# Optimization experiments

Hardware: AMD Instinct MI355X
Metric: run time of the kernel (lower is better)

Reference implementation:

```python
import jax, jax.numpy as jnp
import numpy as np

HEADS = 8

def setup_inputs() -> dict:
    key = jax.random.key(0)
    ks = jax.random.split(key, 10)
    B, S, E = 2, 2048, 512
    q = jax.random.normal(ks[0], (B, S, E), jnp.float32)
    k = jax.random.normal(ks[1], (B, S, E), jnp.float32)
    v = jax.random.normal(ks[2], (B, S, E), jnp.float32)
    mask = jnp.zeros((S, S), jnp.float32)  # additive mask [s_q, s_k]
    scale = 0.02
    Wq = jax.random.normal(ks[3], (E, E), jnp.float32) * scale
    bq = jax.random.normal(ks[4], (E,), jnp.float32) * scale
    Wk = jax.random.normal(ks[5], (E, E), jnp.float32) * scale
    bk = jax.random.normal(ks[6], (E,), jnp.float32) * scale
    Wv = jax.random.normal(ks[7], (E, E), jnp.float32) * scale
    bv = jax.random.normal(ks[8], (E,), jnp.float32) * scale
    return {"q": q, "k": k, "v": v, "mask": mask,
            "Wq": Wq, "bq": bq, "Wk": Wk, "bk": bk, "Wv": Wv, "bv": bv}

def reference(q, k, v, mask, Wq, bq, Wk, bk, Wv, bv):
    H = HEADS
    b, s_q, _ = q.shape
    s_k = k.shape[1]
    s_v = v.shape[1]
    # NOTE: faithful to source: row-major view(b, H, s, -1) WITHOUT transposing
    # seq/head axes first (quirk of the original module).
    K = jnp.swapaxes((k @ Wk.T + bk).reshape(b, H, s_k, -1), 2, 3)  # [b,H,dh,s_k]
    Q = (q @ Wq.T + bq).reshape(b, H, s_q, -1)                      # [b,H,s_q,dh]
    V = (v @ Wv.T + bv).reshape(b, H, s_v, -1)                      # [b,H,s_v,dh]
    # NOTE: original scales by sqrt(K.shape[-1]) AFTER the transpose, i.e. sqrt(s_k)
    scores = (Q @ K) / jnp.sqrt(jnp.asarray(s_k, jnp.float32))      # [b,H,s_q,s_k]
    scores = scores + mask[:s_q, :s_k]
    attn = jax.nn.softmax(scores, axis=-1)
    out = (attn @ V).reshape(b, s_q, -1)  # [b, s_q, e]
    return out
```

## Files before the change

kernel.cpp:

```cpp
#include <hip/hip_runtime.h>


#define SEQ 2048
#define EMB 512
#define DH  64
#define MROWS 4096
#define NROWS 32768

typedef float  v4f __attribute__((ext_vector_type(4)));
typedef short  v8s __attribute__((ext_vector_type(8)));
typedef __fp16 v2h __attribute__((ext_vector_type(2)));

static __device__ __forceinline__ unsigned int f2bf(float f) {
    unsigned int u = __float_as_uint(f);
    u += 0x7fffu + ((u >> 16) & 1u);
    return u >> 16;
}
static __device__ __forceinline__ unsigned int pack2(float a, float b) {
    return f2bf(a) | (f2bf(b) << 16);
}
static __device__ __forceinline__ unsigned int packh2(float a, float b) {
    v2h h = __builtin_amdgcn_cvt_pkrtz(a, b);
    return __builtin_bit_cast(unsigned int, h);
}

__global__ __launch_bounds__(256, 3) void proj_kernel(
    const float* __restrict__ q, const float* __restrict__ k, const float* __restrict__ v,
    const float* __restrict__ Wq, const float* __restrict__ bq,
    const float* __restrict__ Wk, const float* __restrict__ bk,
    const float* __restrict__ Wv, const float* __restrict__ bv,
    const float* __restrict__ mask,
    unsigned short* __restrict__ Qbf, unsigned short* __restrict__ Kbf,
    unsigned short* __restrict__ Vbf, float* __restrict__ maskT)
{
    const int tid = threadIdx.x;

    if (blockIdx.x >= 768) {
        const int mb2 = blockIdx.x - 768;
        const int rb = mb2 >> 5, kt = mb2 & 31;
        float* tile = maskT + ((size_t)rb * 32 + kt) * 8192;
#pragma unroll
        for (int i = 0; i < 8; ++i) {
            int s = tid + i * 256;
            int l  = s & 63;
            int cb = (s >> 6) & 3;
            int g  = (s >> 8) & 1;
            int w  = (s >> 9) & 3;
            int qd = l >> 4, n = l & 15;
            float4 f = *(const float4*)&mask[
                (size_t)(rb * 128 + w * 32 + g * 16 + n) * SEQ + kt * 64 + cb * 16 + qd * 4];
            *(float4*)&tile[(size_t)s * 4] = f;
        }
        return;
    }

    __shared__ __align__(16) char smem[27648];
    char* As = smem;
    char* Ws = smem + 9216;

    const int id  = blockIdx.x;
    const int pos = id & 31;
    const int nb  = pos >> 3;
    const int unit = (id >> 5) * 8 + (pos & 7);
    const int mb = unit & 63;
    const int z  = unit >> 6;

    const float* A    = (z == 0) ? q  : (z == 1) ? k  : v;
    const float* W    = (z == 0) ? Wq : (z == 1) ? Wk : Wv;
    const float* bias = (z == 0) ? bq : (z == 1) ? bk : bv;
    unsigned short* Cg = (z == 0) ? Qbf : (z == 1) ? Kbf : Vbf;

    const int w    = tid >> 6;
    const int lane = tid & 63;
    const int qd   = lane >> 4;
    const int n    = lane & 15;
    const int m0 = mb * 64, n0 = nb * 128;

    float4 areg[4], wreg[8];
#pragma unroll
    for (int i = 0; i < 4; ++i) {
        int c = tid + i * 256;
        areg[i] = *(const float4*)&A[(size_t)(m0 + (c >> 4)) * EMB + (c & 15) * 4];
    }
#pragma unroll
    for (int i = 0; i < 8; ++i) {
        int c = tid + i * 256;
        wreg[i] = *(const float4*)&W[(size_t)(n0 + (c >> 4)) * EMB + (c & 15) * 4];
    }

    v4f acc[8];
#pragma unroll
    for (int cb = 0; cb < 8; ++cb) acc[cb] = (v4f)0.f;

#pragma unroll 1
    for (int kt = 0; kt < 8; ++kt) {
        __syncthreads();
#pragma unroll
        for (int i = 0; i < 4; ++i) {
            int c = tid + i * 256;
            uint2 pk = { pack2(areg[i].x, areg[i].y), pack2(areg[i].z, areg[i].w) };
            *(uint2*)&As[(c >> 4) * 144 + (c & 15) * 8] = pk;
        }
#pragma unroll
        for (int i = 0; i < 8; ++i) {
            int c = tid + i * 256;
            uint2 pk = { pack2(wreg[i].x, wreg[i].y), pack2(wreg[i].z, wreg[i].w) };
            *(uint2*)&Ws[(c >> 4) * 144 + (c & 15) * 8] = pk;
        }
        __syncthreads();

        if (kt + 1 < 8) {
#pragma unroll
            for (int i = 0; i < 4; ++i) {
                int c = tid + i * 256;
                areg[i] = *(const float4*)&A[(size_t)(m0 + (c >> 4)) * EMB + (kt+1) * 64 + (c & 15) * 4];
            }
#pragma unroll
            for (int i = 0; i < 8; ++i) {
                int c = tid + i * 256;
                wreg[i] = *(const float4*)&W[(size_t)(n0 + (c >> 4)) * EMB + (kt+1) * 64 + (c & 15) * 4];
            }
        }

#pragma unroll
        for (int ks = 0; ks < 2; ++ks) {
            v8s af = *(const v8s*)&As[(w * 16 + n) * 144 + ks * 64 + qd * 16];
#pragma unroll
            for (int cb = 0; cb < 8; ++cb) {
                v8s bfr = *(const v8s*)&Ws[(cb * 16 + n) * 144 + ks * 64 + qd * 16];
                acc[cb] = __builtin_amdgcn_mfma_f32_16x16x32_bf16(af, bfr, acc[cb], 0, 0, 0);
            }
        }
    }

    const float osc = (z == 0) ? 0.02209708691207961f : 1.0f;
    float bb[8];
#pragma unroll
    for (int cb = 0; cb < 8; ++cb) bb[cb] = bias[n0 + cb * 16 + n];
#pragma unroll
    for (int cb = 0; cb < 8; ++cb)
#pragma unroll
        for (int r = 0; r < 4; ++r) acc[cb][r] = (acc[cb][r] + bb[cb]) * osc;

    __syncthreads();
    short* Ct = (short*)smem;
#pragma unroll
    for (int cb = 0; cb < 8; ++cb)
#pragma unroll
        for (int r = 0; r < 4; ++r)
            Ct[(w * 16 + qd * 4 + r) * 136 + cb * 16 + n] = (short)f2bf(acc[cb][r]);
    __syncthreads();
    const int rr = tid >> 2, q4 = tid & 3;
#pragma unroll
    for (int i = 0; i < 4; ++i) {
        uint4 t4 = *(const uint4*)&smem[rr * 272 + q4 * 64 + i * 16];
        *(uint4*)&Cg[(size_t)(m0 + rr) * EMB + n0 + q4 * 32 + i * 8] = t4;
    }
}

__global__ __launch_bounds__(256) void vtrans_kernel(
    const unsigned short* __restrict__ Vbf, unsigned short* __restrict__ VtT)
{
    __shared__ unsigned short T[64 * 136];
    const int bh = blockIdx.x, kt = blockIdx.y;
    const int tid = threadIdx.x;
    const unsigned short* Vh = Vbf + (size_t)bh * (SEQ * DH) + (size_t)kt * 64 * DH;
#pragma unroll
    for (int i = 0; i < 2; ++i) {
        int c = tid + i * 256;
        int s_l = c >> 3, ch = c & 7;
        uint4 t4 = *(const uint4*)&Vh[c * 8];
        const unsigned short* e = (const unsigned short*)&t4;
#pragma unroll
        for (int j = 0; j < 8; ++j)
            T[(ch * 8 + j) * 136 + s_l] = e[j];
    }
    __syncthreads();
    unsigned short* Ot = VtT + ((size_t)bh * 32 + kt) * (64 * 64);
    const int d = tid >> 2, sq = tid & 3;
#pragma unroll
    for (int i = 0; i < 2; ++i) {
        uint4 t4 = *(const uint4*)&T[d * 136 + sq * 16 + i * 8];
        *(uint4*)&Ot[d * 64 + sq * 16 + i * 8] = t4;
    }
}

template <int SPLITS>
__global__ __launch_bounds__(256, 4) void attn_kernel(
    const unsigned short* __restrict__ Qbf, const unsigned short* __restrict__ Kbf,
    const unsigned short* __restrict__ VtT,
    const float* __restrict__ maskT, const float* __restrict__ maskf,
    unsigned short* __restrict__ Opart, float* __restrict__ ml,
    float* __restrict__ out)
{
    __shared__ __align__(16) char smem[36864];
    char* Ks  = smem;
    char* Vts = smem + 9216;

    const int tid  = threadIdx.x;
    const int w    = tid >> 6;
    const int lane = tid & 63;
    const int qd   = lane >> 4;
    const int n    = lane & 15;
    char* Ps = smem + 18432 + w * 4608;

    const int id = blockIdx.x;
    const int rb = ((id >> 3) & 1) * 8 + (id & 7);
    const int bh = (id >> 4) & 15;
    const int kq = id >> 8;
    const int KT0 = kq * (32 / SPLITS), KT1 = KT0 + 32 / SPLITS;

    const unsigned short* Qh = Qbf + (size_t)bh * (SEQ * DH);
    const unsigned short* Kh = Kbf + (size_t)bh * (SEQ * DH);
    const unsigned short* Vth = VtT + (size_t)bh * 32 * 4096;

    v8s qf[2][2];
#pragma unroll
    for (int g = 0; g < 2; ++g) {
        const size_t qrow = (size_t)(rb * 128 + w * 32 + g * 16 + n);
#pragma unroll
        for (int ks = 0; ks < 2; ++ks)
            qf[g][ks] = *(const v8s*)&Qh[qrow * DH + ks * 32 + qd * 8];
    }

    uint4 kreg[2], vreg[2];
#pragma unroll
    for (int p = 0; p < 2; ++p) {
        int c = tid + p * 256;
        kreg[p] = *(const uint4*)&Kh[(size_t)KT0 * 4096 + c * 8];
        vreg[p] = *(const uint4*)&Vth[(size_t)KT0 * 4096 + c * 8];
    }

    float l_[2] = { 0.f, 0.f };
    v4f oacc[2][4];
#pragma unroll
    for (int g = 0; g < 2; ++g)
#pragma unroll
        for (int cb = 0; cb < 4; ++cb) oacc[g][cb] = (v4f)0.f;

#pragma unroll 1
    for (int kt = KT0; kt < KT1; ++kt) {
        __syncthreads();
#pragma unroll
        for (int p = 0; p < 2; ++p) {
            int c = tid + p * 256;
            *(uint4*)&Ks [(c >> 3) * 144 + (c & 7) * 16] = kreg[p];
            *(uint4*)&Vts[(c >> 3) * 144 + (c & 7) * 16] = vreg[p];
        }
        __syncthreads();

        v4f sacc[2][4];
        float4 mk[2][4];
        if (SPLITS > 1) {
            const float* tileF = maskT + ((size_t)rb * 32 + kt) * 8192;
#pragma unroll
            for (int g = 0; g < 2; ++g)
#pragma unroll
                for (int cb = 0; cb < 4; ++cb)
                    sacc[g][cb] = *(const v4f*)&tileF[
                        (size_t)((((w * 2 + g) * 4 + cb) * 64) + qd * 16 + n) * 4];
        } else {
#pragma unroll
            for (int g = 0; g < 2; ++g) {
                const size_t mrow = (size_t)(rb * 128 + w * 32 + g * 16 + n);
#pragma unroll
                for (int cb = 0; cb < 4; ++cb) {
                    mk[g][cb] = *(const float4*)&maskf[mrow * SEQ + kt * 64 + cb * 16 + qd * 4];
                    sacc[g][cb] = (v4f)0.f;
                }
            }
        }

        if (kt + 1 < KT1) {
#pragma unroll
            for (int p = 0; p < 2; ++p) {
                int c = tid + p * 256;
                kreg[p] = *(const uint4*)&Kh[(size_t)(kt + 1) * 4096 + c * 8];
                vreg[p] = *(const uint4*)&Vth[(size_t)(kt + 1) * 4096 + c * 8];
            }
        }

#pragma unroll
        for (int ks = 0; ks < 2; ++ks)
#pragma unroll
            for (int cb = 0; cb < 4; ++cb) {
                v8s kf = *(const v8s*)&Ks[(cb * 16 + n) * 144 + ks * 64 + qd * 16];
#pragma unroll
                for (int g = 0; g < 2; ++g)
                    sacc[g][cb] = __builtin_amdgcn_mfma_f32_16x16x32_bf16(kf, qf[g][ks], sacc[g][cb], 0, 0, 0);
            }

#pragma unroll
        for (int g = 0; g < 2; ++g) {
            float rs = 0.f;
            float pv[4][4];
#pragma unroll
            for (int cb = 0; cb < 4; ++cb) {
                if (SPLITS == 1) {
                    sacc[g][cb][0] += mk[g][cb].x; sacc[g][cb][1] += mk[g][cb].y;
                    sacc[g][cb][2] += mk[g][cb].z; sacc[g][cb][3] += mk[g][cb].w;
                }
#pragma unroll
                for (int r = 0; r < 4; ++r) {
                    float e = __expf(sacc[g][cb][r]);
                    pv[cb][r] = e;
                    rs += e;
                }
            }
            rs += __shfl_xor(rs, 16);
            rs += __shfl_xor(rs, 32);
            l_[g] += rs;
#pragma unroll
            for (int cb = 0; cb < 4; ++cb) {
                uint2 pk = { pack2(pv[cb][0], pv[cb][1]), pack2(pv[cb][2], pv[cb][3]) };
                *(uint2*)&Ps[(g * 16 + n) * 144 + cb * 32 + qd * 8] = pk;
            }
        }

#pragma unroll
        for (int ks = 0; ks < 2; ++ks) {
            v8s pf[2];
#pragma unroll
            for (int g = 0; g < 2; ++g)
                pf[g] = *(const v8s*)&Ps[(g * 16 + n) * 144 + ks * 64 + qd * 16];
#pragma unroll
            for (int cb = 0; cb < 4; ++cb) {
                v8s vf = *(const v8s*)&Vts[(cb * 16 + n) * 144 + ks * 64 + qd * 16];
#pragma unroll
                for (int g = 0; g < 2; ++g)
                    oacc[g][cb] = __builtin_amdgcn_mfma_f32_16x16x32_bf16(vf, pf[g], oacc[g][cb], 0, 0, 0);
            }
        }
    }

    if (SPLITS == 1) {
#pragma unroll
        for (int g = 0; g < 2; ++g) {
            const float inv = 1.0f / l_[g];
#pragma unroll
            for (int cb = 0; cb < 4; ++cb)
#pragma unroll
                for (int r = 0; r < 4; ++r) oacc[g][cb][r] *= inv;
        }
    } else {
        if (qd == 0) {
#pragma unroll
            for (int g = 0; g < 2; ++g) {
                const size_t row = (size_t)bh * SEQ + rb * 128 + w * 32 + g * 16 + n;
                ml[(size_t)kq * NROWS + row] = l_[g];
            }
        }
    }
    __syncthreads();
#pragma unroll
    for (int g = 0; g < 2; ++g)
#pragma unroll
        for (int cb = 0; cb < 4; ++cb)
            *(v4f*)&smem[(w * 32 + g * 16 + n) * 272 + cb * 64 + qd * 16] = oacc[g][cb];
    __syncthreads();
    const int r_l = tid >> 1, hf = tid & 1;
    if (SPLITS == 1) {
        float* dst = &out[((size_t)bh * SEQ + rb * 128 + r_l) * DH + hf * 32];
#pragma unroll
        for (int i = 0; i < 8; ++i) {
            float4 t4 = *(const float4*)&smem[r_l * 272 + hf * 128 + i * 16];
            *(float4*)&dst[i * 4] = t4;
        }
    } else {
        unsigned short* dst = &Opart[((size_t)kq * NROWS + (size_t)bh * SEQ + rb * 128 + r_l) * DH + hf * 32];
#pragma unroll
        for (int i = 0; i < 4; ++i) {
            float4 f0 = *(const float4*)&smem[r_l * 272 + hf * 128 + i * 32];
            float4 f1 = *(const float4*)&smem[r_l * 272 + hf * 128 + i * 32 + 16];
            uint4 o = { packh2(f0.x, f0.y), packh2(f0.z, f0.w),
                        packh2(f1.x, f1.y), packh2(f1.z, f1.w) };
            *(uint4*)&dst[i * 8] = o;
        }
    }
}

__global__ __launch_bounds__(256) void combine_kernel(
    const unsigned int* __restrict__ Opart, const float* __restrict__ ml,
    float* __restrict__ out, int splits)
{
    const int tid = threadIdx.x;
    const size_t row = (size_t)blockIdx.x * 16 + (tid >> 4);
    const int d4 = (tid & 15) * 4;
    float denom = 0.f;
    float4 o = make_float4(0.f, 0.f, 0.f, 0.f);
    for (int s = 0; s < splits; ++s) {
        denom += ml[(size_t)s * NROWS + row];
        uint2 u = *(const uint2*)&Opart[((size_t)s * NROWS + row) * 32 + (d4 >> 1)];
        v2h h0 = __builtin_bit_cast(v2h, u.x);
        v2h h1 = __builtin_bit_cast(v2h, u.y);
        o.x += (float)h0.x; o.y += (float)h0.y;
        o.z += (float)h1.x; o.w += (float)h1.y;
    }
    const float inv = 1.0f / denom;
    o.x *= inv; o.y *= inv; o.z *= inv; o.w *= inv;
    *(float4*)&out[row * DH + d4] = o;
}

extern "C" void kernel_launch(void* const* d_in, const int* in_sizes, int n_in,
                              void* d_out, int out_size, void* d_ws, size_t ws_size,
                              hipStream_t stream) {
    const float* q    = (const float*)d_in[0];
    const float* k    = (const float*)d_in[1];
    const float* v    = (const float*)d_in[2];
    const float* mask = (const float*)d_in[3];
    const float* Wq   = (const float*)d_in[4];
    const float* bq   = (const float*)d_in[5];
    const float* Wk   = (const float*)d_in[6];
    const float* bk   = (const float*)d_in[7];
    const float* Wv   = (const float*)d_in[8];
    const float* bv   = (const float*)d_in[9];

    char* ws = (char*)d_ws;
    const size_t MB = 1024 * 1024;
    unsigned short* Qbf   = (unsigned short*)(ws + 0);
    unsigned short* Kbf   = (unsigned short*)(ws + 4 * MB);
    unsigned short* VtT   = (unsigned short*)(ws + 8 * MB);
    unsigned short* Opart = (unsigned short*)(ws + 12 * MB);
    unsigned short* Vbf   = (unsigned short*)(ws + 12 * MB);
    float*          mlp   = (float*)(ws + 28 * MB);
    float*          maskT = (float*)(ws + 29 * MB);

    const size_t need_split = 45 * MB;
    const bool do_split = ws_size >= need_split;

    if (do_split) {
        proj_kernel<<<1280, 256, 0, stream>>>(q, k, v, Wq, bq, Wk, bk, Wv, bv,
                                              mask, Qbf, Kbf, Vbf, maskT);
        dim3 tgrid(16, 32);
        vtrans_kernel<<<tgrid, 256, 0, stream>>>(Vbf, VtT);
        attn_kernel<4><<<1024, 256, 0, stream>>>(Qbf, Kbf, VtT, maskT, mask,
                                                 Opart, mlp, (float*)d_out);
        combine_kernel<<<NROWS / 16, 256, 0, stream>>>((const unsigned int*)Opart,
                                                       mlp, (float*)d_out, 4);
    } else {
        proj_kernel<<<768, 256, 0, stream>>>(q, k, v, Wq, bq, Wk, bk, Wv, bv,
                                             mask, Qbf, Kbf, Vbf, maskT);
        dim3 tgrid(16, 32);
        vtrans_kernel<<<tgrid, 256, 0, stream>>>(Vbf, VtT);
        attn_kernel<1><<<256, 256, 0, stream>>>(Qbf, Kbf, VtT, maskT, mask,
                                                Opart, mlp, (float*)d_out);
    }
}
```

Baseline: 180.6 us.

## Pass P through ds_bpermute instead of LDS and halve shared memory

Softmax probabilities are now moved from the S-accumulator layout into the MFMA B-operand layout with ds_bpermute lane shuffles, so the per-wave P buffer in shared memory is no longer needed. The output epilogue is split into two passes over g so that it fits in the smaller buffer. Shared memory use drops from 36 KB to 18 KB and the launch bound rises to 6 blocks per CU to raise occupancy. The cost is eight bpermutes per g and ks, an extra pair of barriers in the epilogue, and tighter register limits that may cause spills.

```diff
diff --git a/kernel.cpp b/kernel.cpp
--- a/kernel.cpp
+++ b/kernel.cpp
@@ -186,14 +186,14 @@
 }
 
 template <int SPLITS>
-__global__ __launch_bounds__(256, 4) void attn_kernel(
+__global__ __launch_bounds__(256, 6) void attn_kernel(
     const unsigned short* __restrict__ Qbf, const unsigned short* __restrict__ Kbf,
     const unsigned short* __restrict__ VtT,
     const float* __restrict__ maskT, const float* __restrict__ maskf,
     unsigned short* __restrict__ Opart, float* __restrict__ ml,
     float* __restrict__ out)
 {
-    __shared__ __align__(16) char smem[36864];
+    __shared__ __align__(16) char smem[18432];
     char* Ks  = smem;
     char* Vts = smem + 9216;
 
@@ -202,7 +202,6 @@
     const int lane = tid & 63;
     const int qd   = lane >> 4;
     const int n    = lane & 15;
-    char* Ps = smem + 18432 + w * 4608;
 
     const int id = blockIdx.x;
     const int rb = ((id >> 3) & 1) * 8 + (id & 7);
@@ -214,6 +213,10 @@
     const unsigned short* Kh = Kbf + (size_t)bh * (SEQ * DH);
     const unsigned short* Vth = VtT + (size_t)bh * 32 * 4096;
 
+    const int aL1 = ((((2 * qd) & 3) * 16) + n) * 4;
+    const int aL2 = ((((2 * qd + 1) & 3) * 16) + n) * 4;
+    const bool hi = (qd >= 2);
+
     v8s qf[2][2];
 #pragma unroll
     for (int g = 0; g < 2; ++g) {
@@ -290,6 +293,7 @@
                     sacc[g][cb] = __builtin_amdgcn_mfma_f32_16x16x32_bf16(kf, qf[g][ks], sacc[g][cb], 0, 0, 0);
             }
 
+        v8s pf[2][2];
 #pragma unroll
         for (int g = 0; g < 2; ++g) {
             float rs = 0.f;
@@ -310,27 +314,38 @@
             rs += __shfl_xor(rs, 16);
             rs += __shfl_xor(rs, 32);
             l_[g] += rs;
-#pragma unroll
-            for (int cb = 0; cb < 4; ++cb) {
-                uint2 pk = { pack2(pv[cb][0], pv[cb][1]), pack2(pv[cb][2], pv[cb][3]) };
-                *(uint2*)&Ps[(g * 16 + n) * 144 + cb * 32 + qd * 8] = pk;
-            }
-        }
-
-#pragma unroll
-        for (int ks = 0; ks < 2; ++ks) {
-            v8s pf[2];
-#pragma unroll
-            for (int g = 0; g < 2; ++g)
-                pf[g] = *(const v8s*)&Ps[(g * 16 + n) * 144 + ks * 64 + qd * 16];
+
+            uint2 pk[4];
+#pragma unroll
+            for (int cb = 0; cb < 4; ++cb)
+                pk[cb] = (uint2){ pack2(pv[cb][0], pv[cb][1]), pack2(pv[cb][2], pv[cb][3]) };
+
+#pragma unroll
+            for (int ks = 0; ks < 2; ++ks) {
+                const int c0 = ks * 2, c1 = ks * 2 + 1;
+                int a0 = __builtin_amdgcn_ds_bpermute(aL1, (int)pk[c0].x);
+                int b0 = __builtin_amdgcn_ds_bpermute(aL1, (int)pk[c1].x);
+                int a1 = __builtin_amdgcn_ds_bpermute(aL1, (int)pk[c0].y);
+                int b1 = __builtin_amdgcn_ds_bpermute(aL1, (int)pk[c1].y);
+                int a2 = __builtin_amdgcn_ds_bpermute(aL2, (int)pk[c0].x);
+                int b2 = __builtin_amdgcn_ds_bpermute(aL2, (int)pk[c1].x);
+                int a3 = __builtin_amdgcn_ds_bpermute(aL2, (int)pk[c0].y);
+                int b3 = __builtin_amdgcn_ds_bpermute(aL2, (int)pk[c1].y);
+                uint4 u = { (unsigned)(hi ? b0 : a0), (unsigned)(hi ? b1 : a1),
+                            (unsigned)(hi ? b2 : a2), (unsigned)(hi ? b3 : a3) };
+                pf[g][ks] = __builtin_bit_cast(v8s, u);
+            }
+        }
+
+#pragma unroll
+        for (int ks = 0; ks < 2; ++ks)
 #pragma unroll
             for (int cb = 0; cb < 4; ++cb) {
                 v8s vf = *(const v8s*)&Vts[(cb * 16 + n) * 144 + ks * 64 + qd * 16];
 #pragma unroll
                 for (int g = 0; g < 2; ++g)
-                    oacc[g][cb] = __builtin_amdgcn_mfma_f32_16x16x32_bf16(vf, pf[g], oacc[g][cb], 0, 0, 0);
-            }
-        }
+                    oacc[g][cb] = __builtin_amdgcn_mfma_f32_16x16x32_bf16(vf, pf[g][ks], oacc[g][cb], 0, 0, 0);
+            }
     }
 
     if (SPLITS == 1) {
@@ -351,30 +366,31 @@
             }
         }
     }
-    __syncthreads();
-#pragma unroll
-    for (int g = 0; g < 2; ++g)
+
+#pragma unroll 1
+    for (int g = 0; g < 2; ++g) {
+        __syncthreads();
 #pragma unroll
         for (int cb = 0; cb < 4; ++cb)
-            *(v4f*)&smem[(w * 32 + g * 16 + n) * 272 + cb * 64 + qd * 16] = oacc[g][cb];
-    __syncthreads();
-    const int r_l = tid >> 1, hf = tid & 1;
-    if (SPLITS == 1) {
-        float* dst = &out[((size_t)bh * SEQ + rb * 128 + r_l) * DH + hf * 32];
-#pragma unroll
-        for (int i = 0; i < 8; ++i) {
-            float4 t4 = *(const float4*)&smem[r_l * 272 + hf * 128 + i * 16];
-            *(float4*)&dst[i * 4] = t4;
-        }
-    } else {
-        unsigned short* dst = &Opart[((size_t)kq * NROWS + (size_t)bh * SEQ + rb * 128 + r_l) * DH + hf * 32];
-#pragma unroll
-        for (int i = 0; i < 4; ++i) {
-            float4 f0 = *(const float4*)&smem[r_l * 272 + hf * 128 + i * 32];
-            float4 f1 = *(const float4*)&smem[r_l * 272 + hf * 128 + i * 32 + 16];
-            uint4 o = { packh2(f0.x, f0.y), packh2(f0.z, f0.w),
-                        packh2(f1.x, f1.y), packh2(f1.z, f1.w) };
-            *(uint4*)&dst[i * 8] = o;
+            *(v4f*)&smem[(w * 16 + n) * 272 + cb * 64 + qd * 16] = oacc[g][cb];
+        __syncthreads();
+        const int r_l = tid >> 2, qq = tid & 3;
+        const int grow = rb * 128 + (r_l >> 4) * 32 + g * 16 + (r_l & 15);
+        if (SPLITS == 1) {
+            float* dst = &out[((size_t)bh * SEQ + grow) * DH + qq * 16];
+#pragma unroll
+            for (int i = 0; i < 4; ++i)
+                *(float4*)&dst[i * 4] = *(const float4*)&smem[r_l * 272 + qq * 64 + i * 16];
+        } else {
+            unsigned short* dst = &Opart[((size_t)kq * NROWS + (size_t)bh * SEQ + grow) * DH + qq * 16];
+#pragma unroll
+            for (int i = 0; i < 2; ++i) {
+                float4 f0 = *(const float4*)&smem[r_l * 272 + qq * 64 + i * 32];
+                float4 f1 = *(const float4*)&smem[r_l * 272 + qq * 64 + i * 32 + 16];
+                uint4 o = { packh2(f0.x, f0.y), packh2(f0.z, f0.w),
+                            packh2(f1.x, f1.y), packh2(f1.z, f1.w) };
+                *(uint4*)&dst[i * 8] = o;
+            }
         }
     }
 }
```

New measurement: 291.8 us. 1.62x slower.
